# Kernel optimization log

Hardware: AMD Instinct MI355X
Metric: run time of the kernel (lower is better)

## Reference

```python
import jax, jax.numpy as jnp
import numpy as np

D = 512
H = 8
DH = D // H
SPK = 4
HG = 128  # max(16, D//4)
EPS = 1e-5


def _layernorm(x, gamma, beta):
    mu = jnp.mean(x, axis=-1, keepdims=True)
    var = jnp.var(x, axis=-1, keepdims=True)
    return (x - mu) * jax.lax.rsqrt(var + EPS) * gamma + beta


def setup_inputs() -> dict:
    key = jax.random.key(0)
    ks = jax.random.split(key, 16)
    B, T = 8, 4096
    s = 0.02
    return {
        'token_emb': jax.random.normal(ks[0], (B, T, D), jnp.float32),
        'speaker_emb': jax.random.normal(ks[1], (B, D), jnp.float32),
        'We': jax.random.normal(ks[2], (D * SPK, D), jnp.float32) * s,
        'be': jnp.zeros((D * SPK,), jnp.float32),
        'spk_pos': jax.random.normal(ks[3], (1, SPK, D), jnp.float32) * s,
        'Wq': jax.random.normal(ks[4], (D, D), jnp.float32) * s,
        'bq': jnp.zeros((D,), jnp.float32),
        'Wk': jax.random.normal(ks[5], (D, D), jnp.float32) * s,
        'bk': jnp.zeros((D,), jnp.float32),
        'Wv': jax.random.normal(ks[6], (D, D), jnp.float32) * s,
        'bv': jnp.zeros((D,), jnp.float32),
        'Wo': jax.random.normal(ks[7], (D, D), jnp.float32) * s,
        'bo': jnp.zeros((D,), jnp.float32),
        'gln_gamma': jnp.ones((D,), jnp.float32),
        'gln_beta': jnp.zeros((D,), jnp.float32),
        'Wg1': jax.random.normal(ks[8], (HG, D), jnp.float32) * s,
        'bg1': jnp.zeros((HG,), jnp.float32),
        'Wg2': jax.random.normal(ks[9], (1, HG), jnp.float32) * s,
        'bg2': jnp.zeros((1,), jnp.float32),
        'ln_gamma': jnp.ones((D,), jnp.float32),
        'ln_beta': jnp.zeros((D,), jnp.float32),
    }


def reference(token_emb, speaker_emb, We, be, spk_pos, Wq, bq, Wk, bk, Wv, bv,
              Wo, bo, gln_gamma, gln_beta, Wg1, bg1, Wg2, bg2, ln_gamma, ln_beta):
    B, T, _ = token_emb.shape
    # speaker expansion: (B,D) -> (B, SPK*D) -> (B,SPK,D), plus learned pos
    spk_tokens = jax.nn.relu(speaker_emb @ We.T + be).reshape(B, SPK, D) + spk_pos
    # multi-head cross-attention (batch_first, eval-mode dropout = identity)
    q = (token_emb @ Wq.T + bq).reshape(B, T, H, DH)
    k = (spk_tokens @ Wk.T + bk).reshape(B, SPK, H, DH)
    v = (spk_tokens @ Wv.T + bv).reshape(B, SPK, H, DH)
    scores = jnp.einsum('bthd,bshd->bhts', q, k) / jnp.sqrt(jnp.float32(DH))
    w = jax.nn.softmax(scores, axis=-1)  # (B,H,T,SPK)
    ctx = jnp.einsum('bhts,bshd->bthd', w, v).reshape(B, T, D)
    attn_output = ctx @ Wo.T + bo
    attn_weights = jnp.mean(w, axis=1)  # torch MHA averages heads -> (B,T,SPK)
    # gate: LN -> Linear -> ReLU -> Linear -> Sigmoid
    g = _layernorm(token_emb, gln_gamma, gln_beta)
    g = jax.nn.relu(g @ Wg1.T + bg1)
    g_used = jax.nn.sigmoid(g @ Wg2.T + bg2)  # (B,T,1)
    # residual + final LayerNorm (dropout identity in eval)
    fused = _layernorm(token_emb + g_used * attn_output, ln_gamma, ln_beta)
    return (fused, attn_weights, g_used)
```

## Files before the change

kernel.cpp:

```cpp
#include <hip/hip_runtime.h>
#include <hip/hip_bf16.h>
#include <stdint.h>

typedef __attribute__((ext_vector_type(8))) short short8;
typedef __attribute__((ext_vector_type(4))) short short4v;
typedef __attribute__((ext_vector_type(4))) float f32x4;
typedef __attribute__((ext_vector_type(2))) unsigned int uint2v;

#define DD 512
#define TT 16
#define TN 4096
#define NB 8

__device__ __forceinline__ unsigned short f2bf(float f){
  uint32_t u = __float_as_uint(f);
  u += 0x7FFFu + ((u >> 16) & 1u);
  return (unsigned short)(u >> 16);
}
__device__ __forceinline__ float bf2f(unsigned short h){
  return __uint_as_float(((uint32_t)h) << 16);
}


__global__ void prep_spk(const float* __restrict__ se, const float* __restrict__ We,
                         const float* __restrict__ be, const float* __restrict__ spos,
                         float* __restrict__ spk){
  int idx = blockIdx.x * 256 + threadIdx.x;
  int sub = idx & 15; int out = idx >> 4;
  int b = out & 7, od = out >> 3;
  const float* wr = We + (size_t)od * DD + sub * 4;
  const float* sb = se + b * DD + sub * 4;
  float acc = 0.f;
#pragma unroll
  for (int i = 0; i < 8; i++){
    float4 w = *(const float4*)(wr + i * 64);
    float4 x = *(const float4*)(sb + i * 64);
    acc += w.x * x.x + w.y * x.y + w.z * x.z + w.w * x.w;
  }
  acc += __shfl_xor(acc, 1); acc += __shfl_xor(acc, 2);
  acc += __shfl_xor(acc, 4); acc += __shfl_xor(acc, 8);
  if (sub == 0) spk[b * 2048 + od] = fmaxf(acc + be[od], 0.f) + spos[od];
}

__global__ void prep_kv(const float* __restrict__ spk, const float* __restrict__ Wk,
                        const float* __restrict__ bk, const float* __restrict__ Wv,
                        const float* __restrict__ bv, float* __restrict__ kb,
                        float* __restrict__ vb){
  int idx = blockIdx.x * 256 + threadIdx.x;
  int sub = idx & 15; int out = idx >> 4;
  int hd = out >> 5; int r = out & 31; int b = r >> 2, s = r & 3;
  const float* sp  = spk + (b * 4 + s) * DD + sub * 4;
  const float* wkr = Wk + (size_t)hd * DD + sub * 4;
  const float* wvr = Wv + (size_t)hd * DD + sub * 4;
  float ak = 0.f, av = 0.f;
#pragma unroll
  for (int i = 0; i < 8; i++){
    float4 x  = *(const float4*)(sp + i * 64);
    float4 wk = *(const float4*)(wkr + i * 64);
    float4 wv = *(const float4*)(wvr + i * 64);
    ak += x.x * wk.x + x.y * wk.y + x.z * wk.z + x.w * wk.w;
    av += x.x * wv.x + x.y * wv.y + x.z * wv.z + x.w * wv.w;
  }
  ak += __shfl_xor(ak, 1); ak += __shfl_xor(ak, 2);
  ak += __shfl_xor(ak, 4); ak += __shfl_xor(ak, 8);
  av += __shfl_xor(av, 1); av += __shfl_xor(av, 2);
  av += __shfl_xor(av, 4); av += __shfl_xor(av, 8);
  if (sub == 0){
    kb[(b * 4 + s) * DD + hd] = ak + bk[hd];
    vb[(b * 4 + s) * DD + hd] = av + bv[hd];
  }
}

__global__ void prep_mu(const float* __restrict__ kb, const float* __restrict__ vb,
                        const float* __restrict__ Wq, const float* __restrict__ bq,
                        const float* __restrict__ Wo, const float* __restrict__ bo,
                        const float* __restrict__ Wg1,
                        const float* __restrict__ glng, const float* __restrict__ glnb,
                        const float* __restrict__ bg1,
                        unsigned short* __restrict__ mS, unsigned short* __restrict__ uS,
                        float* __restrict__ cArr, unsigned short* __restrict__ wg1S,
                        float* __restrict__ e1, float* __restrict__ e2){
  int idx = blockIdx.x * 256 + threadIdx.x;
  if (idx < 131072){
    int d = idx & 511; int j = (idx >> 9) & 31; int b = idx >> 14;
    int h = j >> 2, s = j & 3;
    const float* kr = kb + (b * 4 + s) * DD + h * 64;
    const float* wq = Wq + (size_t)(h * 64) * DD + d;
    float acc = 0.f;
#pragma unroll 16
    for (int dh = 0; dh < 64; dh++) acc += wq[(size_t)dh * DD] * kr[dh];
    int kt = d >> 5, kgp = (d >> 3) & 3, e = d & 7;
    int half = j >> 4;
    mS[(size_t)(b * 16 + kt) * 1024 + half * 512 + (kgp * 16 + (j & 15)) * 8 + e] = f2bf(acc);
  } else if (idx < 262144){
    int t = idx - 131072;
    int j = t & 31; int d = (t >> 5) & 511; int b = t >> 14;
    int h = j >> 2, s = j & 3;
    const float* vr = vb + (b * 4 + s) * DD + h * 64;
    const float* wo = Wo + (size_t)d * DD + h * 64;
    float acc = 0.f;
#pragma unroll 8
    for (int dh = 0; dh < 64; dh += 4){
      float4 v4 = *(const float4*)(vr + dh);
      float4 w4 = *(const float4*)(wo + dh);
      acc += v4.x * w4.x + v4.y * w4.y + v4.z * w4.z + v4.w * w4.w;
    }
    int nc = d >> 7, nt = (d >> 4) & 7, r16p = d & 15;
    int kgp = j >> 3, e = j & 7;
    uS[(size_t)(b * 32 + nc * 8 + nt) * 512 + (kgp * 16 + r16p) * 8 + e] =
        f2bf(acc + bo[d] * 0.125f);
  } else if (idx < 327680){
    int t = idx - 262144;
    int col = t >> 9, d = t & 511;
    int nt = col >> 4, c16 = col & 15;
    int kt = d >> 5, kgp = (d >> 3) & 3, e = d & 7;
    wg1S[(size_t)(nt * 16 + kt) * 512 + (kgp * 16 + c16) * 8 + e] = f2bf(Wg1[t] * glng[d]);
  } else if (idx < 327936){
    int t = idx - 327680; int j = t & 31, b = t >> 5;
    int h = j >> 2, s = j & 3;
    const float* kr = kb + (b * 4 + s) * DD + h * 64;
    const float* bqp = bq + h * 64;
    float acc = 0.f;
    for (int dh = 0; dh < 64; dh++) acc += bqp[dh] * kr[dh];
    cArr[b * 32 + j] = acc;
  } else if (idx < 328064){
    int col = idx - 327936;
    const float* wr = Wg1 + (size_t)col * DD;
    float a1 = 0.f, a2 = 0.f;
    for (int d = 0; d < DD; d += 4){
      float4 w  = *(const float4*)(wr + d);
      float4 gm = *(const float4*)(glng + d);
      float4 bt = *(const float4*)(glnb + d);
      a1 += w.x * gm.x + w.y * gm.y + w.z * gm.z + w.w * gm.w;
      a2 += w.x * bt.x + w.y * bt.y + w.z * bt.z + w.w * bt.w;
    }
    e1[col] = a1; e2[col] = a2 + bg1[col];
  }
}


__global__ __launch_bounds__(256, 4) void fused_main(
    const float* __restrict__ xin,
    const float* __restrict__ e1v, const float* __restrict__ e2v,
    const float* __restrict__ wg2v, const float* __restrict__ bg2v,
    const float* __restrict__ lng, const float* __restrict__ lnb,
    const unsigned short* __restrict__ mS,
    const unsigned short* __restrict__ uS,
    const float* __restrict__ cArr,
    const unsigned short* __restrict__ wg1S,
    float* __restrict__ outF, float* __restrict__ outAW, float* __restrict__ outG)
{
  __shared__ __align__(16) unsigned short Yb[TT * DD];
  __shared__ __align__(16) unsigned short Wl[TT * 32];
  __shared__ float smu[TT], srs[TT];
  __shared__ float aws[2][64];
  __shared__ float gp[4][TT];
  __shared__ float pp[4][TT], qq[4][TT];

  const int tid  = threadIdx.x;
  const int w    = tid >> 6;
  const int lane = tid & 63;
  const int r16  = lane & 15;
  const int kg   = lane >> 4;
  const int bb   = blockIdx.x >> 8;
  const int t0   = (blockIdx.x & 255) << 4;
  const size_t rowbase = (size_t)bb * TN + t0;
  const int swzS = (r16 & 7) << 3;

  const float* xbase = xin + rowbase * DD;
#pragma unroll
  for (int i = 0; i < 4; ++i){
    const int rr = w * 4 + i;
    const int swz = (rr & 7) << 3;
    float s = 0.f, q = 0.f;
#pragma unroll
    for (int h2 = 0; h2 < 2; ++h2){
      const int col = h2 * 256 + lane * 4;
      float4 v4 = *(const float4*)(xbase + rr * DD + col);
      float xv[4] = {v4.x, v4.y, v4.z, v4.w};
      short4v pk;
#pragma unroll
      for (int j = 0; j < 4; ++j){ s += xv[j]; q += xv[j]*xv[j]; pk[j] = (short)f2bf(xv[j]); }
      *(short4v*)&Yb[rr * DD + (col ^ swz)] = pk;
    }
#pragma unroll
    for (int off = 1; off < 64; off <<= 1){ s += __shfl_xor(s, off); q += __shfl_xor(q, off); }
    if (lane == 0){
      const float mu = s * (1.f/DD);
      smu[rr] = mu;
      srs[rr] = rsqrtf(q * (1.f/DD) - mu*mu + 1e-5f);
    }
  }
  __syncthreads();

  const int half = w & 1;
  const int nt0 = w * 2;
  const unsigned short* mSp  = mS + (size_t)bb * 16384 + half * 512 + lane * 8;
  const unsigned short* wgp0 = wg1S + (size_t)(nt0 * 16) * 512 + lane * 8;
  const unsigned short* wgp1 = wgp0 + (size_t)16 * 512;
  f32x4 sa = {0.f,0.f,0.f,0.f}, ga0 = {0.f,0.f,0.f,0.f}, ga1 = {0.f,0.f,0.f,0.f};
  if (w < 2){
#pragma unroll
    for (int kt = 0; kt < 16; ++kt){
      short8 af = *(const short8*)&Yb[r16 * DD + ((kt*32 + kg*8) ^ swzS)];
      short8 b0 = *(const short8*)(mSp + (size_t)kt * 1024);
      sa  = __builtin_amdgcn_mfma_f32_16x16x32_bf16(af, b0, sa, 0, 0, 0);
      short8 wf0 = *(const short8*)(wgp0 + (size_t)kt * 512);
      ga0 = __builtin_amdgcn_mfma_f32_16x16x32_bf16(wf0, af, ga0, 0, 0, 0);
      short8 wf1 = *(const short8*)(wgp1 + (size_t)kt * 512);
      ga1 = __builtin_amdgcn_mfma_f32_16x16x32_bf16(wf1, af, ga1, 0, 0, 0);
    }
  } else {
#pragma unroll
    for (int kt = 0; kt < 16; ++kt){
      short8 af = *(const short8*)&Yb[r16 * DD + ((kt*32 + kg*8) ^ swzS)];
      short8 wf0 = *(const short8*)(wgp0 + (size_t)kt * 512);
      ga0 = __builtin_amdgcn_mfma_f32_16x16x32_bf16(wf0, af, ga0, 0, 0, 0);
      short8 wf1 = *(const short8*)(wgp1 + (size_t)kt * 512);
      ga1 = __builtin_amdgcn_mfma_f32_16x16x32_bf16(wf1, af, ga1, 0, 0, 0);
    }
  }

  float4 e1c[2], e2c[2], w2c[2];
#pragma unroll
  for (int t = 0; t < 2; ++t){
    const int c4 = (nt0 + t) * 16 + kg * 4;
    e1c[t] = *(const float4*)(e1v + c4);
    e2c[t] = *(const float4*)(e2v + c4);
    w2c[t] = *(const float4*)(wg2v + c4);
  }
  float4 lgh[2], lbh[2];
#pragma unroll
  for (int h2 = 0; h2 < 2; ++h2){
    lgh[h2] = *(const float4*)(lng + h2*256 + lane*4);
    lbh[h2] = *(const float4*)(lnb + h2*256 + lane*4);
  }
  const float bg2s = bg2v[0];

  if (w < 2){
    const float cv = cArr[bb*32 + half*16 + r16];
#pragma unroll
    for (int r = 0; r < 4; ++r){
      float s0 = (sa[r] + cv) * 0.125f;
      float mx = fmaxf(s0, __shfl_xor(s0, 1)); mx = fmaxf(mx, __shfl_xor(mx, 2));
      float e0 = __expf(s0 - mx);
      float d0 = e0; d0 += __shfl_xor(d0, 1); d0 += __shfl_xor(d0, 2);
      float wv = e0 / d0;
      float t = wv; t += __shfl_xor(t, 4); t += __shfl_xor(t, 8);
      const int rw = kg * 4 + r;
      Wl[rw * 32 + half * 16 + r16] = f2bf(wv);
      if ((lane & 12) == 0) aws[half][rw * 4 + (lane & 3)] = t;
    }
  }

  {
    const float mu_t = smu[r16], rs_t = srs[r16];
    float part = 0.f;
#pragma unroll
    for (int t = 0; t < 2; ++t){
      const f32x4 ga = t ? ga1 : ga0;
      float ea[4] = {e1c[t].x, e1c[t].y, e1c[t].z, e1c[t].w};
      float eb[4] = {e2c[t].x, e2c[t].y, e2c[t].z, e2c[t].w};
      float wc[4] = {w2c[t].x, w2c[t].y, w2c[t].z, w2c[t].w};
#pragma unroll
      for (int r = 0; r < 4; ++r){
        float gv = rs_t * (ga[r] - mu_t * ea[r]) + eb[r];
        part += fmaxf(gv, 0.f) * wc[r];
      }
    }
    part += __shfl_xor(part, 16); part += __shfl_xor(part, 32);
    if (kg == 0) gp[w][r16] = part;
  }
  __syncthreads();

  if (w == 2){
    const int tok = lane >> 2;
    const float val = (aws[0][lane] + aws[1][lane]) * 0.125f;
    outAW[(rowbase + tok) * 4 + (lane & 3)] = val;
  }
  float g_reg;
  {
    const float gs = gp[0][r16] + gp[1][r16] + gp[2][r16] + gp[3][r16];
    g_reg = 1.f / (1.f + __expf(-(gs + bg2s)));
    if (w == 3 && kg == 0) outG[rowbase + r16] = g_reg;
  }

  short8 awf = *(const short8*)&Wl[r16 * 32 + kg * 8];
  const unsigned short* uSp = uS + (size_t)bb * 16384 + (size_t)(w * 8) * 512 + lane * 8;
  f32x4 acc[8];
#pragma unroll
  for (int nt = 0; nt < 8; ++nt){
    short8 uf = *(const short8*)(uSp + (size_t)nt * 512);
    f32x4 z = {0.f,0.f,0.f,0.f};
    acc[nt] = __builtin_amdgcn_mfma_f32_16x16x32_bf16(uf, awf, z, 0, 0, 0);
  }
  float psum = 0.f, psq = 0.f;
#pragma unroll
  for (int nt = 0; nt < 8; ++nt){
    const int c4 = w * 128 + nt * 16 + kg * 4;
    const int idx = r16 * DD + (c4 ^ swzS);
    uint2v xch = *(const uint2v*)&Yb[idx];
    unsigned int lo = xch[0], hi = xch[1];
    float y0 = bf2f((unsigned short)(lo & 0xffffu)) + g_reg * acc[nt][0];
    float y1 = bf2f((unsigned short)(lo >> 16))     + g_reg * acc[nt][1];
    float y2 = bf2f((unsigned short)(hi & 0xffffu)) + g_reg * acc[nt][2];
    float y3 = bf2f((unsigned short)(hi >> 16))     + g_reg * acc[nt][3];
    psum += (y0 + y1) + (y2 + y3);
    psq  += (y0*y0 + y1*y1) + (y2*y2 + y3*y3);
    uint2v yp;
    yp[0] = (unsigned)f2bf(y0) | ((unsigned)f2bf(y1) << 16);
    yp[1] = (unsigned)f2bf(y2) | ((unsigned)f2bf(y3) << 16);
    *(uint2v*)&Yb[idx] = yp;
  }
  psum += __shfl_xor(psum, 16); psum += __shfl_xor(psum, 32);
  psq  += __shfl_xor(psq, 16);  psq  += __shfl_xor(psq, 32);
  if (kg == 0){ pp[w][r16] = psum; qq[w][r16] = psq; }
  __syncthreads();

#pragma unroll
  for (int i = 0; i < 4; ++i){
    const int rr = w * 4 + i;
    const float sm = pp[0][rr] + pp[1][rr] + pp[2][rr] + pp[3][rr];
    const float sq = qq[0][rr] + qq[1][rr] + qq[2][rr] + qq[3][rr];
    const float mu2 = sm * (1.f/DD);
    const float rs2 = rsqrtf(sq * (1.f/DD) - mu2*mu2 + 1e-5f);
    const int swz = (rr & 7) << 3;
#pragma unroll
    for (int h2 = 0; h2 < 2; ++h2){
      const int col = h2 * 256 + lane * 4;
      short4v yv = *(const short4v*)&Yb[rr * DD + (col ^ swz)];
      float la[4] = {lgh[h2].x, lgh[h2].y, lgh[h2].z, lgh[h2].w};
      float lb4[4] = {lbh[h2].x, lbh[h2].y, lbh[h2].z, lbh[h2].w};
      float4 o;
      o.x = (bf2f((unsigned short)yv[0]) - mu2) * rs2 * la[0] + lb4[0];
      o.y = (bf2f((unsigned short)yv[1]) - mu2) * rs2 * la[1] + lb4[1];
      o.z = (bf2f((unsigned short)yv[2]) - mu2) * rs2 * la[2] + lb4[2];
      o.w = (bf2f((unsigned short)yv[3]) - mu2) * rs2 * la[3] + lb4[3];
      *(float4*)(outF + (rowbase + rr) * DD + col) = o;
    }
  }
}


extern "C" void kernel_launch(void* const* d_in, const int* in_sizes, int n_in,
                              void* d_out, int out_size, void* d_ws, size_t ws_size,
                              hipStream_t stream)
{
  const float* token = (const float*)d_in[0];
  const float* semb  = (const float*)d_in[1];
  const float* We    = (const float*)d_in[2];
  const float* be    = (const float*)d_in[3];
  const float* spos  = (const float*)d_in[4];
  const float* Wq    = (const float*)d_in[5];
  const float* bq    = (const float*)d_in[6];
  const float* Wk    = (const float*)d_in[7];
  const float* bk    = (const float*)d_in[8];
  const float* Wv    = (const float*)d_in[9];
  const float* bv    = (const float*)d_in[10];
  const float* Wo    = (const float*)d_in[11];
  const float* bo    = (const float*)d_in[12];
  const float* glng  = (const float*)d_in[13];
  const float* glnb  = (const float*)d_in[14];
  const float* Wg1   = (const float*)d_in[15];
  const float* bg1   = (const float*)d_in[16];
  const float* Wg2   = (const float*)d_in[17];
  const float* bg2   = (const float*)d_in[18];
  const float* lng   = (const float*)d_in[19];
  const float* lnb   = (const float*)d_in[20];

  char* ws = (char*)d_ws;
  float* e1             = (float*)(ws + 0);
  float* e2             = (float*)(ws + 512);
  float* spk            = (float*)(ws + 0);
  float* kb             = (float*)(ws + 65536);
  float* vb             = (float*)(ws + 131072);
  unsigned short* mS    = (unsigned short*)(ws + 196608);
  unsigned short* uS    = (unsigned short*)(ws + 458752);
  float* cArr           = (float*)(ws + 720896);
  unsigned short* wg1S  = (unsigned short*)(ws + 721920);

  float* outF  = (float*)d_out;
  float* outAW = outF + (size_t)NB * TN * DD;
  float* outG  = outAW + (size_t)NB * TN * 4;

  prep_spk<<<dim3(1024), dim3(256), 0, stream>>>(semb, We, be, spos, spk);
  prep_kv<<<dim3(1024), dim3(256), 0, stream>>>(spk, Wk, bk, Wv, bv, kb, vb);
  prep_mu<<<dim3(1282), dim3(256), 0, stream>>>(kb, vb, Wq, bq, Wo, bo, Wg1, glng, glnb, bg1,
                                                mS, uS, cArr, wg1S, e1, e2);
  fused_main<<<dim3(NB * TN / TT), dim3(256), 0, stream>>>(
      token, e1, e2, Wg2, bg2, lng, lnb,
      mS, uS, cArr, wg1S, outF, outAW, outG);
}
```

Baseline: 68.51 us.

## Process two token tiles per block with register prefetch and packed bf16 conversion

Each block of the fused kernel now handles two consecutive 16-token tiles, halving the grid. The next tile's input rows are loaded into registers while the current tile is being processed, and the shared bf16 staging buffer is double-buffered. Manual float-to-bf16 rounding is replaced by the packed `v_cvt_pk_bf16_f32` instruction. The aim is to hide global load latency and reduce per-block setup, at the cost of more registers and LDS per block, which could hurt occupancy or cause spills under the 256x4 launch bound.

```diff
diff --git a/kernel.cpp b/kernel.cpp
--- a/kernel.cpp
+++ b/kernel.cpp
@@ -9,6 +9,7 @@
 
 #define DD 512
 #define TT 16
+#define TILES 2
 #define TN 4096
 #define NB 8
 
@@ -19,6 +20,11 @@
 }
 __device__ __forceinline__ float bf2f(unsigned short h){
   return __uint_as_float(((uint32_t)h) << 16);
+}
+__device__ __forceinline__ unsigned cvtpk(float a, float b){
+  unsigned r;
+  asm("v_cvt_pk_bf16_f32 %0, %1, %2" : "=v"(r) : "v"(a), "v"(b));
+  return r;
 }
 
 
@@ -150,10 +156,10 @@
     const unsigned short* __restrict__ wg1S,
     float* __restrict__ outF, float* __restrict__ outAW, float* __restrict__ outG)
 {
-  __shared__ __align__(16) unsigned short Yb[TT * DD];
+  __shared__ __align__(16) unsigned short Yb[2][TT * DD];
   __shared__ __align__(16) unsigned short Wl[TT * 32];
   __shared__ float smu[TT], srs[TT];
-  __shared__ float aws[2][64];
+  __shared__ float aws[2][TT * 4];
   __shared__ float gp[4][TT];
   __shared__ float pp[4][TT], qq[4][TT];
 
@@ -162,181 +168,207 @@
   const int lane = tid & 63;
   const int r16  = lane & 15;
   const int kg   = lane >> 4;
-  const int bb   = blockIdx.x >> 8;
-  const int t0   = (blockIdx.x & 255) << 4;
-  const size_t rowbase = (size_t)bb * TN + t0;
+  const int bb   = blockIdx.x >> 7;
+  const int pairTok = (blockIdx.x & 127) << 5;
   const int swzS = (r16 & 7) << 3;
 
-  const float* xbase = xin + rowbase * DD;
-#pragma unroll
-  for (int i = 0; i < 4; ++i){
-    const int rr = w * 4 + i;
-    const int swz = (rr & 7) << 3;
-    float s = 0.f, q = 0.f;
-#pragma unroll
-    for (int h2 = 0; h2 < 2; ++h2){
-      const int col = h2 * 256 + lane * 4;
-      float4 v4 = *(const float4*)(xbase + rr * DD + col);
-      float xv[4] = {v4.x, v4.y, v4.z, v4.w};
-      short4v pk;
-#pragma unroll
-      for (int j = 0; j < 4; ++j){ s += xv[j]; q += xv[j]*xv[j]; pk[j] = (short)f2bf(xv[j]); }
-      *(short4v*)&Yb[rr * DD + (col ^ swz)] = pk;
-    }
-#pragma unroll
-    for (int off = 1; off < 64; off <<= 1){ s += __shfl_xor(s, off); q += __shfl_xor(q, off); }
-    if (lane == 0){
-      const float mu = s * (1.f/DD);
-      smu[rr] = mu;
-      srs[rr] = rsqrtf(q * (1.f/DD) - mu*mu + 1e-5f);
-    }
-  }
-  __syncthreads();
-
   const int half = w & 1;
-  const int nt0 = w * 2;
+  const int nt0  = w * 2;
   const unsigned short* mSp  = mS + (size_t)bb * 16384 + half * 512 + lane * 8;
   const unsigned short* wgp0 = wg1S + (size_t)(nt0 * 16) * 512 + lane * 8;
   const unsigned short* wgp1 = wgp0 + (size_t)16 * 512;
-  f32x4 sa = {0.f,0.f,0.f,0.f}, ga0 = {0.f,0.f,0.f,0.f}, ga1 = {0.f,0.f,0.f,0.f};
-  if (w < 2){
-#pragma unroll
-    for (int kt = 0; kt < 16; ++kt){
-      short8 af = *(const short8*)&Yb[r16 * DD + ((kt*32 + kg*8) ^ swzS)];
-      short8 b0 = *(const short8*)(mSp + (size_t)kt * 1024);
-      sa  = __builtin_amdgcn_mfma_f32_16x16x32_bf16(af, b0, sa, 0, 0, 0);
-      short8 wf0 = *(const short8*)(wgp0 + (size_t)kt * 512);
-      ga0 = __builtin_amdgcn_mfma_f32_16x16x32_bf16(wf0, af, ga0, 0, 0, 0);
-      short8 wf1 = *(const short8*)(wgp1 + (size_t)kt * 512);
-      ga1 = __builtin_amdgcn_mfma_f32_16x16x32_bf16(wf1, af, ga1, 0, 0, 0);
-    }
-  } else {
-#pragma unroll
-    for (int kt = 0; kt < 16; ++kt){
-      short8 af = *(const short8*)&Yb[r16 * DD + ((kt*32 + kg*8) ^ swzS)];
-      short8 wf0 = *(const short8*)(wgp0 + (size_t)kt * 512);
-      ga0 = __builtin_amdgcn_mfma_f32_16x16x32_bf16(wf0, af, ga0, 0, 0, 0);
-      short8 wf1 = *(const short8*)(wgp1 + (size_t)kt * 512);
-      ga1 = __builtin_amdgcn_mfma_f32_16x16x32_bf16(wf1, af, ga1, 0, 0, 0);
-    }
-  }
-
-  float4 e1c[2], e2c[2], w2c[2];
-#pragma unroll
-  for (int t = 0; t < 2; ++t){
-    const int c4 = (nt0 + t) * 16 + kg * 4;
-    e1c[t] = *(const float4*)(e1v + c4);
-    e2c[t] = *(const float4*)(e2v + c4);
-    w2c[t] = *(const float4*)(wg2v + c4);
-  }
-  float4 lgh[2], lbh[2];
-#pragma unroll
-  for (int h2 = 0; h2 < 2; ++h2){
-    lgh[h2] = *(const float4*)(lng + h2*256 + lane*4);
-    lbh[h2] = *(const float4*)(lnb + h2*256 + lane*4);
-  }
-  const float bg2s = bg2v[0];
-
-  if (w < 2){
-    const float cv = cArr[bb*32 + half*16 + r16];
-#pragma unroll
-    for (int r = 0; r < 4; ++r){
-      float s0 = (sa[r] + cv) * 0.125f;
-      float mx = fmaxf(s0, __shfl_xor(s0, 1)); mx = fmaxf(mx, __shfl_xor(mx, 2));
-      float e0 = __expf(s0 - mx);
-      float d0 = e0; d0 += __shfl_xor(d0, 1); d0 += __shfl_xor(d0, 2);
-      float wv = e0 / d0;
-      float t = wv; t += __shfl_xor(t, 4); t += __shfl_xor(t, 8);
-      const int rw = kg * 4 + r;
-      Wl[rw * 32 + half * 16 + r16] = f2bf(wv);
-      if ((lane & 12) == 0) aws[half][rw * 4 + (lane & 3)] = t;
-    }
-  }
-
+  const unsigned short* uSp  = uS + (size_t)bb * 16384 + (size_t)(w * 8) * 512 + lane * 8;
+  const float cv = cArr[bb * 32 + half * 16 + r16];
+
+  float4 xs[8];
   {
-    const float mu_t = smu[r16], rs_t = srs[r16];
-    float part = 0.f;
-#pragma unroll
-    for (int t = 0; t < 2; ++t){
-      const f32x4 ga = t ? ga1 : ga0;
-      float ea[4] = {e1c[t].x, e1c[t].y, e1c[t].z, e1c[t].w};
-      float eb[4] = {e2c[t].x, e2c[t].y, e2c[t].z, e2c[t].w};
-      float wc[4] = {w2c[t].x, w2c[t].y, w2c[t].z, w2c[t].w};
+    const float* xb = xin + ((size_t)bb * TN + pairTok) * DD;
+#pragma unroll
+    for (int i = 0; i < 4; ++i)
+#pragma unroll
+      for (int h2 = 0; h2 < 2; ++h2)
+        xs[i * 2 + h2] = *(const float4*)(xb + (w * 4 + i) * DD + h2 * 256 + lane * 4);
+  }
+
+#pragma unroll
+  for (int t = 0; t < TILES; ++t){
+    unsigned short* Ybc = Yb[t & 1];
+    const size_t rowbase = (size_t)bb * TN + pairTok + t * TT;
+
+#pragma unroll
+    for (int i = 0; i < 4; ++i){
+      const int rr = w * 4 + i;
+      const int swz = (rr & 7) << 3;
+      float s = 0.f, q = 0.f;
+#pragma unroll
+      for (int h2 = 0; h2 < 2; ++h2){
+        float4 v4 = xs[i * 2 + h2];
+        s += (v4.x + v4.y) + (v4.z + v4.w);
+        q += (v4.x*v4.x + v4.y*v4.y) + (v4.z*v4.z + v4.w*v4.w);
+        uint2v pk;
+        pk[0] = cvtpk(v4.x, v4.y);
+        pk[1] = cvtpk(v4.z, v4.w);
+        const int col = h2 * 256 + lane * 4;
+        *(uint2v*)&Ybc[rr * DD + (col ^ swz)] = pk;
+      }
+#pragma unroll
+      for (int off = 1; off < 64; off <<= 1){ s += __shfl_xor(s, off); q += __shfl_xor(q, off); }
+      if (lane == 0){
+        const float mu = s * (1.f/DD);
+        smu[rr] = mu;
+        srs[rr] = rsqrtf(q * (1.f/DD) - mu*mu + 1e-5f);
+      }
+    }
+
+    if (t + 1 < TILES){
+      const float* xb = xin + (rowbase + TT) * DD;
+#pragma unroll
+      for (int i = 0; i < 4; ++i)
+#pragma unroll
+        for (int h2 = 0; h2 < 2; ++h2)
+          xs[i * 2 + h2] = *(const float4*)(xb + (w * 4 + i) * DD + h2 * 256 + lane * 4);
+    }
+    __syncthreads();
+
+    f32x4 sa = {0.f,0.f,0.f,0.f}, ga0 = {0.f,0.f,0.f,0.f}, ga1 = {0.f,0.f,0.f,0.f};
+    if (w < 2){
+#pragma unroll
+      for (int kt = 0; kt < 16; ++kt){
+        short8 af = *(const short8*)&Ybc[r16 * DD + ((kt*32 + kg*8) ^ swzS)];
+        short8 b0 = *(const short8*)(mSp + (size_t)kt * 1024);
+        sa  = __builtin_amdgcn_mfma_f32_16x16x32_bf16(af, b0, sa, 0, 0, 0);
+        short8 wf0 = *(const short8*)(wgp0 + (size_t)kt * 512);
+        ga0 = __builtin_amdgcn_mfma_f32_16x16x32_bf16(wf0, af, ga0, 0, 0, 0);
+        short8 wf1 = *(const short8*)(wgp1 + (size_t)kt * 512);
+        ga1 = __builtin_amdgcn_mfma_f32_16x16x32_bf16(wf1, af, ga1, 0, 0, 0);
+      }
+    } else {
+#pragma unroll
+      for (int kt = 0; kt < 16; ++kt){
+        short8 af = *(const short8*)&Ybc[r16 * DD + ((kt*32 + kg*8) ^ swzS)];
+        short8 wf0 = *(const short8*)(wgp0 + (size_t)kt * 512);
+        ga0 = __builtin_amdgcn_mfma_f32_16x16x32_bf16(wf0, af, ga0, 0, 0, 0);
+        short8 wf1 = *(const short8*)(wgp1 + (size_t)kt * 512);
+        ga1 = __builtin_amdgcn_mfma_f32_16x16x32_bf16(wf1, af, ga1, 0, 0, 0);
+      }
+    }
+
+    float4 e1c[2], e2c[2], w2c[2];
+#pragma unroll
+    for (int tt2 = 0; tt2 < 2; ++tt2){
+      const int c4 = (nt0 + tt2) * 16 + kg * 4;
+      e1c[tt2] = *(const float4*)(e1v + c4);
+      e2c[tt2] = *(const float4*)(e2v + c4);
+      w2c[tt2] = *(const float4*)(wg2v + c4);
+    }
+    float4 lgh[2], lbh[2];
+#pragma unroll
+    for (int h2 = 0; h2 < 2; ++h2){
+      lgh[h2] = *(const float4*)(lng + h2*256 + lane*4);
+      lbh[h2] = *(const float4*)(lnb + h2*256 + lane*4);
+    }
+    const float bg2s = bg2v[0];
+
+    if (w < 2){
 #pragma unroll
       for (int r = 0; r < 4; ++r){
-        float gv = rs_t * (ga[r] - mu_t * ea[r]) + eb[r];
-        part += fmaxf(gv, 0.f) * wc[r];
-      }
-    }
-    part += __shfl_xor(part, 16); part += __shfl_xor(part, 32);
-    if (kg == 0) gp[w][r16] = part;
-  }
-  __syncthreads();
-
-  if (w == 2){
-    const int tok = lane >> 2;
-    const float val = (aws[0][lane] + aws[1][lane]) * 0.125f;
-    outAW[(rowbase + tok) * 4 + (lane & 3)] = val;
-  }
-  float g_reg;
-  {
-    const float gs = gp[0][r16] + gp[1][r16] + gp[2][r16] + gp[3][r16];
-    g_reg = 1.f / (1.f + __expf(-(gs + bg2s)));
-    if (w == 3 && kg == 0) outG[rowbase + r16] = g_reg;
-  }
-
-  short8 awf = *(const short8*)&Wl[r16 * 32 + kg * 8];
-  const unsigned short* uSp = uS + (size_t)bb * 16384 + (size_t)(w * 8) * 512 + lane * 8;
-  f32x4 acc[8];
-#pragma unroll
-  for (int nt = 0; nt < 8; ++nt){
-    short8 uf = *(const short8*)(uSp + (size_t)nt * 512);
-    f32x4 z = {0.f,0.f,0.f,0.f};
-    acc[nt] = __builtin_amdgcn_mfma_f32_16x16x32_bf16(uf, awf, z, 0, 0, 0);
-  }
-  float psum = 0.f, psq = 0.f;
-#pragma unroll
-  for (int nt = 0; nt < 8; ++nt){
-    const int c4 = w * 128 + nt * 16 + kg * 4;
-    const int idx = r16 * DD + (c4 ^ swzS);
-    uint2v xch = *(const uint2v*)&Yb[idx];
-    unsigned int lo = xch[0], hi = xch[1];
-    float y0 = bf2f((unsigned short)(lo & 0xffffu)) + g_reg * acc[nt][0];
-    float y1 = bf2f((unsigned short)(lo >> 16))     + g_reg * acc[nt][1];
-    float y2 = bf2f((unsigned short)(hi & 0xffffu)) + g_reg * acc[nt][2];
-    float y3 = bf2f((unsigned short)(hi >> 16))     + g_reg * acc[nt][3];
-    psum += (y0 + y1) + (y2 + y3);
-    psq  += (y0*y0 + y1*y1) + (y2*y2 + y3*y3);
-    uint2v yp;
-    yp[0] = (unsigned)f2bf(y0) | ((unsigned)f2bf(y1) << 16);
-    yp[1] = (unsigned)f2bf(y2) | ((unsigned)f2bf(y3) << 16);
-    *(uint2v*)&Yb[idx] = yp;
-  }
-  psum += __shfl_xor(psum, 16); psum += __shfl_xor(psum, 32);
-  psq  += __shfl_xor(psq, 16);  psq  += __shfl_xor(psq, 32);
-  if (kg == 0){ pp[w][r16] = psum; qq[w][r16] = psq; }
-  __syncthreads();
-
-#pragma unroll
-  for (int i = 0; i < 4; ++i){
-    const int rr = w * 4 + i;
-    const float sm = pp[0][rr] + pp[1][rr] + pp[2][rr] + pp[3][rr];
-    const float sq = qq[0][rr] + qq[1][rr] + qq[2][rr] + qq[3][rr];
-    const float mu2 = sm * (1.f/DD);
-    const float rs2 = rsqrtf(sq * (1.f/DD) - mu2*mu2 + 1e-5f);
-    const int swz = (rr & 7) << 3;
-#pragma unroll
-    for (int h2 = 0; h2 < 2; ++h2){
-      const int col = h2 * 256 + lane * 4;
-      short4v yv = *(const short4v*)&Yb[rr * DD + (col ^ swz)];
-      float la[4] = {lgh[h2].x, lgh[h2].y, lgh[h2].z, lgh[h2].w};
-      float lb4[4] = {lbh[h2].x, lbh[h2].y, lbh[h2].z, lbh[h2].w};
-      float4 o;
-      o.x = (bf2f((unsigned short)yv[0]) - mu2) * rs2 * la[0] + lb4[0];
-      o.y = (bf2f((unsigned short)yv[1]) - mu2) * rs2 * la[1] + lb4[1];
-      o.z = (bf2f((unsigned short)yv[2]) - mu2) * rs2 * la[2] + lb4[2];
-      o.w = (bf2f((unsigned short)yv[3]) - mu2) * rs2 * la[3] + lb4[3];
-      *(float4*)(outF + (rowbase + rr) * DD + col) = o;
+        float s0 = (sa[r] + cv) * 0.125f;
+        float mx = fmaxf(s0, __shfl_xor(s0, 1)); mx = fmaxf(mx, __shfl_xor(mx, 2));
+        float e0 = __expf(s0 - mx);
+        float d0 = e0; d0 += __shfl_xor(d0, 1); d0 += __shfl_xor(d0, 2);
+        float wv = e0 / d0;
+        float ts = wv; ts += __shfl_xor(ts, 4); ts += __shfl_xor(ts, 8);
+        const int rw = kg * 4 + r;
+        Wl[rw * 32 + half * 16 + r16] = f2bf(wv);
+        if ((lane & 12) == 0) aws[half][rw * 4 + (lane & 3)] = ts;
+      }
+    }
+
+    {
+      const float mu_t = smu[r16], rs_t = srs[r16];
+      float part = 0.f;
+#pragma unroll
+      for (int tt2 = 0; tt2 < 2; ++tt2){
+        const f32x4 ga = tt2 ? ga1 : ga0;
+        float ea[4] = {e1c[tt2].x, e1c[tt2].y, e1c[tt2].z, e1c[tt2].w};
+        float eb[4] = {e2c[tt2].x, e2c[tt2].y, e2c[tt2].z, e2c[tt2].w};
+        float wc[4] = {w2c[tt2].x, w2c[tt2].y, w2c[tt2].z, w2c[tt2].w};
+#pragma unroll
+        for (int r = 0; r < 4; ++r){
+          float gv = rs_t * (ga[r] - mu_t * ea[r]) + eb[r];
+          part += fmaxf(gv, 0.f) * wc[r];
+        }
+      }
+      part += __shfl_xor(part, 16); part += __shfl_xor(part, 32);
+      if (kg == 0) gp[w][r16] = part;
+    }
+    __syncthreads();
+
+    if (w == 2){
+      const int tok = lane >> 2;
+      const int si = lane & 3;
+      const float val = (aws[0][tok*4 + si] + aws[1][tok*4 + si]) * 0.125f;
+      outAW[(rowbase + tok) * 4 + si] = val;
+    }
+    float g_reg;
+    {
+      const float gs = gp[0][r16] + gp[1][r16] + gp[2][r16] + gp[3][r16];
+      g_reg = 1.f / (1.f + __expf(-(gs + bg2s)));
+      if (w == 3 && kg == 0) outG[rowbase + r16] = g_reg;
+    }
+
+    short8 awf = *(const short8*)&Wl[r16 * 32 + kg * 8];
+    f32x4 acc[8];
+#pragma unroll
+    for (int nt = 0; nt < 8; ++nt){
+      short8 uf = *(const short8*)(uSp + (size_t)nt * 512);
+      f32x4 z = {0.f,0.f,0.f,0.f};
+      acc[nt] = __builtin_amdgcn_mfma_f32_16x16x32_bf16(uf, awf, z, 0, 0, 0);
+    }
+    float psum = 0.f, psq = 0.f;
+#pragma unroll
+    for (int nt = 0; nt < 8; ++nt){
+      const int c4 = w * 128 + nt * 16 + kg * 4;
+      const int idx = r16 * DD + (c4 ^ swzS);
+      uint2v xch = *(const uint2v*)&Ybc[idx];
+      unsigned int lo = xch[0], hi = xch[1];
+      float y0 = bf2f((unsigned short)(lo & 0xffffu)) + g_reg * acc[nt][0];
+      float y1 = bf2f((unsigned short)(lo >> 16))     + g_reg * acc[nt][1];
+      float y2 = bf2f((unsigned short)(hi & 0xffffu)) + g_reg * acc[nt][2];
+      float y3 = bf2f((unsigned short)(hi >> 16))     + g_reg * acc[nt][3];
+      psum += (y0 + y1) + (y2 + y3);
+      psq  += (y0*y0 + y1*y1) + (y2*y2 + y3*y3);
+      uint2v yp;
+      yp[0] = cvtpk(y0, y1);
+      yp[1] = cvtpk(y2, y3);
+      *(uint2v*)&Ybc[idx] = yp;
+    }
+    psum += __shfl_xor(psum, 16); psum += __shfl_xor(psum, 32);
+    psq  += __shfl_xor(psq, 16);  psq  += __shfl_xor(psq, 32);
+    if (kg == 0){ pp[w][r16] = psum; qq[w][r16] = psq; }
+    __syncthreads();
+
+#pragma unroll
+    for (int i = 0; i < 4; ++i){
+      const int rr = w * 4 + i;
+      const float sm = pp[0][rr] + pp[1][rr] + pp[2][rr] + pp[3][rr];
+      const float sq = qq[0][rr] + qq[1][rr] + qq[2][rr] + qq[3][rr];
+      const float mu2 = sm * (1.f/DD);
+      const float rs2 = rsqrtf(sq * (1.f/DD) - mu2*mu2 + 1e-5f);
+      const int swz = (rr & 7) << 3;
+#pragma unroll
+      for (int h2 = 0; h2 < 2; ++h2){
+        const int col = h2 * 256 + lane * 4;
+        short4v yv = *(const short4v*)&Ybc[rr * DD + (col ^ swz)];
+        float la[4] = {lgh[h2].x, lgh[h2].y, lgh[h2].z, lgh[h2].w};
+        float lb4[4] = {lbh[h2].x, lbh[h2].y, lbh[h2].z, lbh[h2].w};
+        float4 o;
+        o.x = (bf2f((unsigned short)yv[0]) - mu2) * rs2 * la[0] + lb4[0];
+        o.y = (bf2f((unsigned short)yv[1]) - mu2) * rs2 * la[1] + lb4[1];
+        o.z = (bf2f((unsigned short)yv[2]) - mu2) * rs2 * la[2] + lb4[2];
+        o.w = (bf2f((unsigned short)yv[3]) - mu2) * rs2 * la[3] + lb4[3];
+        *(float4*)(outF + (rowbase + rr) * DD + col) = o;
+      }
     }
   }
 }
@@ -387,7 +419,7 @@
   prep_kv<<<dim3(1024), dim3(256), 0, stream>>>(spk, Wk, bk, Wv, bv, kb, vb);
   prep_mu<<<dim3(1282), dim3(256), 0, stream>>>(kb, vb, Wq, bq, Wo, bo, Wg1, glng, glnb, bg1,
                                                 mS, uS, cArr, wg1S, e1, e2);
-  fused_main<<<dim3(NB * TN / TT), dim3(256), 0, stream>>>(
+  fused_main<<<dim3(NB * TN / (TT * TILES)), dim3(256), 0, stream>>>(
       token, e1, e2, Wg2, bg2, lng, lnb,
       mS, uS, cArr, wg1S, outF, outAW, outG);
 }
```

New measurement: 93.64 us. 1.37x slower.

## Vectorize Wq-k projection and software-pipeline operand loads in main kernel

Applied to the files above, without the earlier changes.

In the prep kernel, each thread of the Wq·k projection now computes four adjacent output columns using float4 loads and writes them as one short4 store. This cuts that branch's thread count and index arithmetic, so the grid shrinks. In the main kernel, all x rows are loaded into registers before the LayerNorm statistics pass. The 16-step MFMA loop now uses a 4-deep register prefetch ring for the LDS and global operands, and the uS fragments are loaded up front. The aim is to hide memory latency behind MFMA work, at the cost of higher register pressure, which could reduce occupancy under the launch bounds.

```diff
diff --git a/kernel.cpp b/kernel.cpp
--- a/kernel.cpp
+++ b/kernel.cpp
@@ -81,19 +81,29 @@
                         float* __restrict__ cArr, unsigned short* __restrict__ wg1S,
                         float* __restrict__ e1, float* __restrict__ e2){
   int idx = blockIdx.x * 256 + threadIdx.x;
-  if (idx < 131072){
-    int d = idx & 511; int j = (idx >> 9) & 31; int b = idx >> 14;
+  if (idx < 32768){
+    int dc = idx & 127, j = (idx >> 7) & 31, b = idx >> 12;
     int h = j >> 2, s = j & 3;
+    const int d0 = dc * 4;
     const float* kr = kb + (b * 4 + s) * DD + h * 64;
-    const float* wq = Wq + (size_t)(h * 64) * DD + d;
-    float acc = 0.f;
-#pragma unroll 16
-    for (int dh = 0; dh < 64; dh++) acc += wq[(size_t)dh * DD] * kr[dh];
-    int kt = d >> 5, kgp = (d >> 3) & 3, e = d & 7;
-    int half = j >> 4;
-    mS[(size_t)(b * 16 + kt) * 1024 + half * 512 + (kgp * 16 + (j & 15)) * 8 + e] = f2bf(acc);
-  } else if (idx < 262144){
-    int t = idx - 131072;
+    const float* wqb = Wq + (size_t)(h * 64) * DD + d0;
+    float4 acc = {0.f, 0.f, 0.f, 0.f};
+#pragma unroll 8
+    for (int dh = 0; dh < 64; ++dh){
+      float4 w4 = *(const float4*)(wqb + (size_t)dh * DD);
+      float kvv = kr[dh];
+      acc.x += kvv * w4.x; acc.y += kvv * w4.y;
+      acc.z += kvv * w4.z; acc.w += kvv * w4.w;
+    }
+    const int kt = d0 >> 5, kgp = (d0 >> 3) & 3, e0 = d0 & 7, half = j >> 4;
+    unsigned short* dst = mS + (size_t)(b * 16 + kt) * 1024 + half * 512 +
+                          (kgp * 16 + (j & 15)) * 8 + e0;
+    short4v st;
+    st[0] = (short)f2bf(acc.x); st[1] = (short)f2bf(acc.y);
+    st[2] = (short)f2bf(acc.z); st[3] = (short)f2bf(acc.w);
+    *(short4v*)dst = st;
+  } else if (idx < 163840){
+    int t = idx - 32768;
     int j = t & 31; int d = (t >> 5) & 511; int b = t >> 14;
     int h = j >> 2, s = j & 3;
     const float* vr = vb + (b * 4 + s) * DD + h * 64;
@@ -109,22 +119,22 @@
     int kgp = j >> 3, e = j & 7;
     uS[(size_t)(b * 32 + nc * 8 + nt) * 512 + (kgp * 16 + r16p) * 8 + e] =
         f2bf(acc + bo[d] * 0.125f);
-  } else if (idx < 327680){
-    int t = idx - 262144;
+  } else if (idx < 229376){
+    int t = idx - 163840;
     int col = t >> 9, d = t & 511;
     int nt = col >> 4, c16 = col & 15;
     int kt = d >> 5, kgp = (d >> 3) & 3, e = d & 7;
     wg1S[(size_t)(nt * 16 + kt) * 512 + (kgp * 16 + c16) * 8 + e] = f2bf(Wg1[t] * glng[d]);
-  } else if (idx < 327936){
-    int t = idx - 327680; int j = t & 31, b = t >> 5;
+  } else if (idx < 229632){
+    int t = idx - 229376; int j = t & 31, b = t >> 5;
     int h = j >> 2, s = j & 3;
     const float* kr = kb + (b * 4 + s) * DD + h * 64;
     const float* bqp = bq + h * 64;
     float acc = 0.f;
     for (int dh = 0; dh < 64; dh++) acc += bqp[dh] * kr[dh];
     cArr[b * 32 + j] = acc;
-  } else if (idx < 328064){
-    int col = idx - 327936;
+  } else if (idx < 229760){
+    int col = idx - 229632;
     const float* wr = Wg1 + (size_t)col * DD;
     float a1 = 0.f, a2 = 0.f;
     for (int d = 0; d < DD; d += 4){
@@ -153,7 +163,7 @@
   __shared__ __align__(16) unsigned short Yb[TT * DD];
   __shared__ __align__(16) unsigned short Wl[TT * 32];
   __shared__ float smu[TT], srs[TT];
-  __shared__ float aws[2][64];
+  __shared__ float aws[2][TT * 4];
   __shared__ float gp[4][TT];
   __shared__ float pp[4][TT], qq[4][TT];
 
@@ -168,6 +178,13 @@
   const int swzS = (r16 & 7) << 3;
 
   const float* xbase = xin + rowbase * DD;
+  float4 xl[8];
+#pragma unroll
+  for (int i = 0; i < 4; ++i)
+#pragma unroll
+    for (int h2 = 0; h2 < 2; ++h2)
+      xl[i * 2 + h2] = *(const float4*)(xbase + (w * 4 + i) * DD + h2 * 256 + lane * 4);
+
 #pragma unroll
   for (int i = 0; i < 4; ++i){
     const int rr = w * 4 + i;
@@ -175,12 +192,13 @@
     float s = 0.f, q = 0.f;
 #pragma unroll
     for (int h2 = 0; h2 < 2; ++h2){
+      float4 v4 = xl[i * 2 + h2];
+      short4v pk;
+      pk[0] = (short)f2bf(v4.x); pk[1] = (short)f2bf(v4.y);
+      pk[2] = (short)f2bf(v4.z); pk[3] = (short)f2bf(v4.w);
+      s += (v4.x + v4.y) + (v4.z + v4.w);
+      q += (v4.x*v4.x + v4.y*v4.y) + (v4.z*v4.z + v4.w*v4.w);
       const int col = h2 * 256 + lane * 4;
-      float4 v4 = *(const float4*)(xbase + rr * DD + col);
-      float xv[4] = {v4.x, v4.y, v4.z, v4.w};
-      short4v pk;
-#pragma unroll
-      for (int j = 0; j < 4; ++j){ s += xv[j]; q += xv[j]*xv[j]; pk[j] = (short)f2bf(xv[j]); }
       *(short4v*)&Yb[rr * DD + (col ^ swz)] = pk;
     }
 #pragma unroll
@@ -194,31 +212,40 @@
   __syncthreads();
 
   const int half = w & 1;
-  const int nt0 = w * 2;
+  const int nt0  = w * 2;
   const unsigned short* mSp  = mS + (size_t)bb * 16384 + half * 512 + lane * 8;
   const unsigned short* wgp0 = wg1S + (size_t)(nt0 * 16) * 512 + lane * 8;
   const unsigned short* wgp1 = wgp0 + (size_t)16 * 512;
+
   f32x4 sa = {0.f,0.f,0.f,0.f}, ga0 = {0.f,0.f,0.f,0.f}, ga1 = {0.f,0.f,0.f,0.f};
+  short8 afb[4], w0b[4], w1b[4], mb[4];
+#pragma unroll
+  for (int p = 0; p < 4; ++p){
+    afb[p] = *(const short8*)&Yb[r16 * DD + ((p*32 + kg*8) ^ swzS)];
+    w0b[p] = *(const short8*)(wgp0 + (size_t)p * 512);
+    w1b[p] = *(const short8*)(wgp1 + (size_t)p * 512);
+  }
   if (w < 2){
 #pragma unroll
-    for (int kt = 0; kt < 16; ++kt){
-      short8 af = *(const short8*)&Yb[r16 * DD + ((kt*32 + kg*8) ^ swzS)];
-      short8 b0 = *(const short8*)(mSp + (size_t)kt * 1024);
-      sa  = __builtin_amdgcn_mfma_f32_16x16x32_bf16(af, b0, sa, 0, 0, 0);
-      short8 wf0 = *(const short8*)(wgp0 + (size_t)kt * 512);
-      ga0 = __builtin_amdgcn_mfma_f32_16x16x32_bf16(wf0, af, ga0, 0, 0, 0);
-      short8 wf1 = *(const short8*)(wgp1 + (size_t)kt * 512);
-      ga1 = __builtin_amdgcn_mfma_f32_16x16x32_bf16(wf1, af, ga1, 0, 0, 0);
-    }
-  } else {
-#pragma unroll
-    for (int kt = 0; kt < 16; ++kt){
-      short8 af = *(const short8*)&Yb[r16 * DD + ((kt*32 + kg*8) ^ swzS)];
-      short8 wf0 = *(const short8*)(wgp0 + (size_t)kt * 512);
-      ga0 = __builtin_amdgcn_mfma_f32_16x16x32_bf16(wf0, af, ga0, 0, 0, 0);
-      short8 wf1 = *(const short8*)(wgp1 + (size_t)kt * 512);
-      ga1 = __builtin_amdgcn_mfma_f32_16x16x32_bf16(wf1, af, ga1, 0, 0, 0);
-    }
+    for (int p = 0; p < 4; ++p) mb[p] = *(const short8*)(mSp + (size_t)p * 1024);
+  }
+
+#pragma unroll
+  for (int kt = 0; kt < 16; ++kt){
+    const int s4 = kt & 3;
+    short8 a  = afb[s4];
+    short8 f0 = w0b[s4];
+    short8 f1 = w1b[s4];
+    short8 bm = mb[s4];
+    if (kt + 4 < 16){
+      afb[s4] = *(const short8*)&Yb[r16 * DD + (((kt+4)*32 + kg*8) ^ swzS)];
+      w0b[s4] = *(const short8*)(wgp0 + (size_t)(kt+4) * 512);
+      w1b[s4] = *(const short8*)(wgp1 + (size_t)(kt+4) * 512);
+      if (w < 2) mb[s4] = *(const short8*)(mSp + (size_t)(kt+4) * 1024);
+    }
+    if (w < 2) sa = __builtin_amdgcn_mfma_f32_16x16x32_bf16(a, bm, sa, 0, 0, 0);
+    ga0 = __builtin_amdgcn_mfma_f32_16x16x32_bf16(f0, a, ga0, 0, 0, 0);
+    ga1 = __builtin_amdgcn_mfma_f32_16x16x32_bf16(f1, a, ga1, 0, 0, 0);
   }
 
   float4 e1c[2], e2c[2], w2c[2];
@@ -275,8 +302,9 @@
 
   if (w == 2){
     const int tok = lane >> 2;
-    const float val = (aws[0][lane] + aws[1][lane]) * 0.125f;
-    outAW[(rowbase + tok) * 4 + (lane & 3)] = val;
+    const int si = lane & 3;
+    const float val = (aws[0][tok*4 + si] + aws[1][tok*4 + si]) * 0.125f;
+    outAW[(rowbase + tok) * 4 + si] = val;
   }
   float g_reg;
   {
@@ -287,12 +315,14 @@
 
   short8 awf = *(const short8*)&Wl[r16 * 32 + kg * 8];
   const unsigned short* uSp = uS + (size_t)bb * 16384 + (size_t)(w * 8) * 512 + lane * 8;
+  short8 uf[8];
+#pragma unroll
+  for (int nt = 0; nt < 8; ++nt) uf[nt] = *(const short8*)(uSp + (size_t)nt * 512);
   f32x4 acc[8];
 #pragma unroll
   for (int nt = 0; nt < 8; ++nt){
-    short8 uf = *(const short8*)(uSp + (size_t)nt * 512);
     f32x4 z = {0.f,0.f,0.f,0.f};
-    acc[nt] = __builtin_amdgcn_mfma_f32_16x16x32_bf16(uf, awf, z, 0, 0, 0);
+    acc[nt] = __builtin_amdgcn_mfma_f32_16x16x32_bf16(uf[nt], awf, z, 0, 0, 0);
   }
   float psum = 0.f, psq = 0.f;
 #pragma unroll
@@ -385,8 +415,8 @@
 
   prep_spk<<<dim3(1024), dim3(256), 0, stream>>>(semb, We, be, spos, spk);
   prep_kv<<<dim3(1024), dim3(256), 0, stream>>>(spk, Wk, bk, Wv, bv, kb, vb);
-  prep_mu<<<dim3(1282), dim3(256), 0, stream>>>(kb, vb, Wq, bq, Wo, bo, Wg1, glng, glnb, bg1,
-                                                mS, uS, cArr, wg1S, e1, e2);
+  prep_mu<<<dim3(898), dim3(256), 0, stream>>>(kb, vb, Wq, bq, Wo, bo, Wg1, glng, glnb, bg1,
+                                               mS, uS, cArr, wg1S, e1, e2);
   fused_main<<<dim3(NB * TN / TT), dim3(256), 0, stream>>>(
       token, e1, e2, Wg2, bg2, lng, lnb,
       mS, uS, cArr, wg1S, outF, outAW, outG);
```

Result: no change. 68.33 us (-0.3%).
